# Performance work log

Measured on AMD Instinct MI355X. Metric: run time of the kernel, lower is better.

The kernel has to match this reference:

```python
import jax, jax.numpy as jnp
import numpy as np

HIDSZ = 256
NAGENTS = 8
NMODELS = 64
NACTIONS = 16
BN = 256  # batch * nagents
IN_DIM = 2 * HIDSZ
INIT_STD = 0.2


def setup_inputs() -> dict:
    key = jax.random.key(0)
    ks = jax.random.split(key, 12)
    inp = jax.random.normal(ks[0], (BN, IN_DIM), jnp.float32)
    prev_hid = jax.random.normal(ks[1], (BN, HIDSZ), jnp.float32)
    comm_in = jax.random.normal(ks[2], (BN, NAGENTS, HIDSZ), jnp.float32)
    agent_ids = jax.random.randint(ks[3], (BN,), 0, NMODELS)
    s = INIT_STD
    params = {
        'enc_w': jax.random.normal(ks[4], (IN_DIM, HIDSZ), jnp.float32) * s,
        'enc_b': jnp.zeros((HIDSZ,), jnp.float32),
        'rnn_w': jax.random.normal(ks[5], (NMODELS, HIDSZ, HIDSZ), jnp.float32) * s,
        'rnn_b': jnp.zeros((NMODELS, HIDSZ), jnp.float32),
        'act_w': jax.random.normal(ks[6], (NMODELS, HIDSZ, NACTIONS), jnp.float32) * s,
        'act_b': jnp.zeros((NMODELS, NACTIONS), jnp.float32),
        'base_w': jax.random.normal(ks[7], (NMODELS, HIDSZ, 1), jnp.float32) * s,
        'base_b': jnp.zeros((NMODELS, 1), jnp.float32),
        'comm_w': jax.random.normal(ks[8], (NMODELS, HIDSZ, HIDSZ * NAGENTS), jnp.float32) * s,
        'comm_b': jnp.zeros((NMODELS, HIDSZ * NAGENTS), jnp.float32),
    }
    return dict(inp=inp, prev_hid=prev_hid, comm_in=comm_in, agent_ids=agent_ids, **params)


def linear_multi(x, w_lut, b_lut, ids):
    # per-example (model-indexed) weight gather + batched matvec
    W = w_lut[ids]            # [BN, in, out]
    b = b_lut[ids]            # [BN, out]
    return jnp.einsum('bi,bio->bo', x, W) + b


def reference(inp, prev_hid, comm_in, agent_ids,
              enc_w, enc_b, rnn_w, rnn_b,
              act_w, act_b, base_w, base_b,
              comm_w, comm_b):
    # __comm2hid: sum over incoming agents (comm_encoder=0 -> identity)
    comm_ = jnp.sum(comm_in, axis=1)                            # [BN, hidsz]
    # _rnn: relu(enc(inp) + rnn_linear(prev_hid, ids) + comm_)
    pre = (inp @ enc_w + enc_b
           + linear_multi(prev_hid, rnn_w, rnn_b, agent_ids)
           + comm_)
    hid = jax.nn.relu(pre)                                      # [BN, hidsz]
    # __action: shared hidden -> policy + baseline
    action_prob = jax.nn.softmax(
        linear_multi(hid, act_w, act_b, agent_ids), axis=-1)    # [BN, nactions]
    baseline = linear_multi(hid, base_w, base_b, agent_ids)     # [BN, 1]
    # __comm_out (fully_connected=True)
    comm_out = linear_multi(hid, comm_w, comm_b, agent_ids)     # [BN, hidsz*nagents]
    return action_prob, baseline, hid, comm_out
```

## Files before the change

### kernel.cpp

```cpp
#include <hip/hip_runtime.h>

#define HIDSZ 256
#define NAGENTS 8
#define NMODELS 64
#define NACTIONS 16
#define BN 256
#define IN_DIM 512
#define COMMSZ 2048

#define OUT_ACT 0
#define OUT_BASE (BN * NACTIONS)
#define OUT_HID (OUT_BASE + BN)
#define OUT_COMM (OUT_HID + BN * HIDSZ)

__global__ void k_sort(const int* __restrict__ ids,
                       int* __restrict__ model_start,
                       int* __restrict__ row_of) {
    __shared__ int cnt[NMODELS];
    __shared__ int base[NMODELS + 1];
    int t = threadIdx.x;
    if (t < NMODELS) cnt[t] = 0;
    __syncthreads();
    int id = ids[t];
    atomicAdd(&cnt[id], 1);
    __syncthreads();
    if (t == 0) {
        int s = 0;
        for (int m = 0; m < NMODELS; ++m) { base[m] = s; s += cnt[m]; }
        base[NMODELS] = s;
    }
    __syncthreads();
    if (t <= NMODELS) model_start[t] = base[t];
    __syncthreads();
    int pos = atomicAdd(&base[id], 1);
    row_of[pos] = t;
}

__global__ __launch_bounds__(256) void k_hid(
    const float* __restrict__ inp, const float* __restrict__ prev_hid,
    const float* __restrict__ comm_in,
    const float* __restrict__ enc_w, const float* __restrict__ enc_b,
    const float* __restrict__ rnn_w, const float* __restrict__ rnn_b,
    const int* __restrict__ model_start, const int* __restrict__ row_of,
    float* __restrict__ out)
{
    int m = blockIdx.x;
    int s = model_start[m];
    int R = model_start[m + 1] - s;
    if (R == 0) return;
    int t = threadIdx.x, lane = t & 63, w = t >> 6;

    __shared__ float4 xs4[4][192];
    __shared__ float red[4][4][HIDSZ];

    for (int g = blockIdx.y; g * 4 < R; g += gridDim.y) {
        __syncthreads();
        {
            int ri = g * 4 + w;
            float4 z4 = make_float4(0.f, 0.f, 0.f, 0.f);
            if (ri < R) {
                int b = row_of[s + ri];
                const float4* ip = (const float4*)(inp + (size_t)b * IN_DIM);
                const float4* ph = (const float4*)(prev_hid + (size_t)b * HIDSZ);
                xs4[w][lane]       = ip[lane];
                xs4[w][64 + lane]  = ip[64 + lane];
                xs4[w][128 + lane] = ph[lane];
            } else {
                xs4[w][lane] = z4; xs4[w][64 + lane] = z4; xs4[w][128 + lane] = z4;
            }
        }
        __syncthreads();

        float acc[4][4];
        #pragma unroll
        for (int r = 0; r < 4; ++r)
            acc[r][0] = acc[r][1] = acc[r][2] = acc[r][3] = 0.f;

        const float* xs = (const float*)xs4;
        const float4* ew4 = (const float4*)enc_w;

        for (int i0 = 0; i0 < 128; i0 += 16) {
            float4 wv[16];
            #pragma unroll
            for (int u = 0; u < 16; ++u)
                wv[u] = ew4[(size_t)(128 * w + i0 + u) * 64 + lane];
            #pragma unroll
            for (int u = 0; u < 16; ++u) {
                int i = 128 * w + i0 + u;
                #pragma unroll
                for (int r = 0; r < 4; ++r) {
                    float x = xs[r * 768 + i];
                    acc[r][0] += x * wv[u].x; acc[r][1] += x * wv[u].y;
                    acc[r][2] += x * wv[u].z; acc[r][3] += x * wv[u].w;
                }
            }
        }
        const float4* rw4 = (const float4*)(rnn_w + (size_t)m * HIDSZ * HIDSZ);
        for (int i0 = 0; i0 < 64; i0 += 16) {
            float4 wv[16];
            #pragma unroll
            for (int u = 0; u < 16; ++u)
                wv[u] = rw4[(size_t)(64 * w + i0 + u) * 64 + lane];
            #pragma unroll
            for (int u = 0; u < 16; ++u) {
                int i = 64 * w + i0 + u;
                #pragma unroll
                for (int r = 0; r < 4; ++r) {
                    float x = xs[r * 768 + 512 + i];
                    acc[r][0] += x * wv[u].x; acc[r][1] += x * wv[u].y;
                    acc[r][2] += x * wv[u].z; acc[r][3] += x * wv[u].w;
                }
            }
        }
        #pragma unroll
        for (int r = 0; r < 4; ++r)
            *(float4*)&red[w][r][lane * 4] =
                make_float4(acc[r][0], acc[r][1], acc[r][2], acc[r][3]);
        __syncthreads();

        int ri = g * 4 + w;
        if (ri < R) {
            int b = row_of[s + ri];
            float4 s0 = *(const float4*)&red[0][w][lane * 4];
            float4 s1 = *(const float4*)&red[1][w][lane * 4];
            float4 s2 = *(const float4*)&red[2][w][lane * 4];
            float4 s3 = *(const float4*)&red[3][w][lane * 4];
            float4 cs = make_float4(0.f, 0.f, 0.f, 0.f);
            const float4* ci = (const float4*)(comm_in + (size_t)b * NAGENTS * HIDSZ);
            #pragma unroll
            for (int a = 0; a < NAGENTS; ++a) {
                float4 v = ci[a * 64 + lane];
                cs.x += v.x; cs.y += v.y; cs.z += v.z; cs.w += v.w;
            }
            float4 eb = ((const float4*)enc_b)[lane];
            float4 rb = ((const float4*)(rnn_b + m * HIDSZ))[lane];
            float4 h;
            h.x = fmaxf(s0.x + s1.x + s2.x + s3.x + cs.x + eb.x + rb.x, 0.f);
            h.y = fmaxf(s0.y + s1.y + s2.y + s3.y + cs.y + eb.y + rb.y, 0.f);
            h.z = fmaxf(s0.z + s1.z + s2.z + s3.z + cs.z + eb.z + rb.z, 0.f);
            h.w = fmaxf(s0.w + s1.w + s2.w + s3.w + cs.w + eb.w + rb.w, 0.f);
            ((float4*)(out + OUT_HID))[(size_t)b * 64 + lane] = h;
        }
    }
}

__global__ __launch_bounds__(256) void k_out(
    const float* __restrict__ act_w, const float* __restrict__ act_b,
    const float* __restrict__ base_w, const float* __restrict__ base_b,
    const float* __restrict__ comm_w, const float* __restrict__ comm_b,
    const int* __restrict__ model_start, const int* __restrict__ row_of,
    float* __restrict__ out)
{
    int m = blockIdx.x, y = blockIdx.y;
    int s = model_start[m];
    int R = model_start[m + 1] - s;
    if (R == 0) return;
    int t = threadIdx.x;
    const float* hid = out + OUT_HID;
    __shared__ float hs[16][HIDSZ];

    if (y == 4) {
        if (blockIdx.z != 0) return;
        const float* aw = act_w + m * HIDSZ * NACTIONS;
        const float* bw = base_w + m * HIDSZ;
        for (int g = 0; g * 16 < R; ++g) {
            __syncthreads();
            for (int k = t; k < 16 * 64; k += 256) {
                int rr = k >> 6, l = k & 63;
                int ri = g * 16 + rr;
                float4 v = make_float4(0.f, 0.f, 0.f, 0.f);
                if (ri < R) v = ((const float4*)(hid + (size_t)row_of[s + ri] * HIDSZ))[l];
                ((float4*)hs)[rr * 64 + l] = v;
            }
            __syncthreads();
            {
                int o = t & 15, rs = t >> 4;
                int ri = g * 16 + rs;
                if (ri < R) {
                    int b = row_of[s + ri];
                    float acc = act_b[m * NACTIONS + o];
                    #pragma unroll 8
                    for (int i = 0; i < HIDSZ; ++i)
                        acc += hs[rs][i] * aw[i * NACTIONS + o];
                    float mx = acc;
                    #pragma unroll
                    for (int d = 1; d < 16; d <<= 1) mx = fmaxf(mx, __shfl_xor(mx, d, 64));
                    float ex = __expf(acc - mx);
                    float sm = ex;
                    #pragma unroll
                    for (int d = 1; d < 16; d <<= 1) sm += __shfl_xor(sm, d, 64);
                    out[OUT_ACT + b * NACTIONS + o] = ex / sm;
                }
            }
            {
                int lane = t & 63, w = t >> 6;
                for (int rr = w; rr < 16; rr += 4) {
                    int ri = g * 16 + rr;
                    if (ri < R) {
                        int b = row_of[s + ri];
                        float p = 0.f;
                        #pragma unroll
                        for (int i = lane; i < HIDSZ; i += 64)
                            p += hs[rr][i] * bw[i];
                        #pragma unroll
                        for (int d = 1; d < 64; d <<= 1) p += __shfl_xor(p, d, 64);
                        if (lane == 0) out[OUT_BASE + b] = p + base_b[m];
                    }
                }
            }
        }
        return;
    }

    int cp = y * 256 + t;
    const float2* cw2 = (const float2*)(comm_w + (size_t)m * HIDSZ * COMMSZ);
    float2 cb = ((const float2*)(comm_b + (size_t)m * COMMSZ))[cp];

    for (int g = blockIdx.z; g * 8 < R; g += gridDim.z) {
        __syncthreads();
        for (int k = t; k < 8 * 64; k += 256) {
            int rr = k >> 6, l = k & 63;
            int ri = g * 8 + rr;
            float4 v = make_float4(0.f, 0.f, 0.f, 0.f);
            if (ri < R) v = ((const float4*)(hid + (size_t)row_of[s + ri] * HIDSZ))[l];
            ((float4*)hs)[rr * 64 + l] = v;
        }
        __syncthreads();

        float acc[8][2];
        #pragma unroll
        for (int r = 0; r < 8; ++r) { acc[r][0] = 0.f; acc[r][1] = 0.f; }

        for (int i0 = 0; i0 < HIDSZ; i0 += 16) {
            float2 wv[16];
            #pragma unroll
            for (int u = 0; u < 16; ++u)
                wv[u] = cw2[(size_t)(i0 + u) * 1024 + cp];
            #pragma unroll
            for (int u = 0; u < 16; ++u) {
                #pragma unroll
                for (int r = 0; r < 8; ++r) {
                    float h = hs[r][i0 + u];
                    acc[r][0] += h * wv[u].x;
                    acc[r][1] += h * wv[u].y;
                }
            }
        }
        #pragma unroll
        for (int r = 0; r < 8; ++r) {
            int ri = g * 8 + r;
            if (ri < R) {
                int b = row_of[s + ri];
                float2 o2;
                o2.x = acc[r][0] + cb.x;
                o2.y = acc[r][1] + cb.y;
                ((float2*)(out + OUT_COMM))[(size_t)b * 1024 + cp] = o2;
            }
        }
    }
}

extern "C" void kernel_launch(void* const* d_in, const int* in_sizes, int n_in,
                              void* d_out, int out_size, void* d_ws, size_t ws_size,
                              hipStream_t stream) {
    const float* inp      = (const float*)d_in[0];
    const float* prev_hid = (const float*)d_in[1];
    const float* comm_in  = (const float*)d_in[2];
    const int*   ids      = (const int*)d_in[3];
    const float* enc_w    = (const float*)d_in[4];
    const float* enc_b    = (const float*)d_in[5];
    const float* rnn_w    = (const float*)d_in[6];
    const float* rnn_b    = (const float*)d_in[7];
    const float* act_w    = (const float*)d_in[8];
    const float* act_b    = (const float*)d_in[9];
    const float* base_w   = (const float*)d_in[10];
    const float* base_b   = (const float*)d_in[11];
    const float* comm_w   = (const float*)d_in[12];
    const float* comm_b   = (const float*)d_in[13];
    float* out = (float*)d_out;

    int* model_start = (int*)d_ws;
    int* row_of      = model_start + 72;

    hipLaunchKernelGGL(k_sort, dim3(1), dim3(256), 0, stream,
                       ids, model_start, row_of);
    hipLaunchKernelGGL(k_hid, dim3(64, 2), dim3(256), 0, stream,
                       inp, prev_hid, comm_in, enc_w, enc_b, rnn_w, rnn_b,
                       model_start, row_of, out);
    hipLaunchKernelGGL(k_out, dim3(64, 5, 2), dim3(256), 0, stream,
                       act_w, act_b, base_w, base_b, comm_w, comm_b,
                       model_start, row_of, out);
}
```

Baseline: 280.2 us.

## Drop sort kernel, build per-model row lists in-block and split hid by column

Removes the single-block sort kernel; each block now scans the 256 agent ids and collects its own model's rows in shared memory. k_hid is restructured so blockIdx.y splits the 256 output columns into two halves instead of splitting row groups. Each thread covers a float2 column pair across 8 rows, and the K dimension is split across 4 waves and reduced through shared memory. This drops one launch and the dependency on the sort kernel, and halves per-block weight traffic in k_hid. The cost is that every block repeats the id scan.

```diff
diff --git a/kernel.cpp b/kernel.cpp
--- a/kernel.cpp
+++ b/kernel.cpp
@@ -6,6 +6,7 @@
 #define NACTIONS 16
 #define BN 256
 #define IN_DIM 512
+#define XDIM 768
 #define COMMSZ 2048
 
 #define OUT_ACT 0
@@ -13,27 +14,14 @@
 #define OUT_HID (OUT_BASE + BN)
 #define OUT_COMM (OUT_HID + BN * HIDSZ)
 
-__global__ void k_sort(const int* __restrict__ ids,
-                       int* __restrict__ model_start,
-                       int* __restrict__ row_of) {
-    __shared__ int cnt[NMODELS];
-    __shared__ int base[NMODELS + 1];
-    int t = threadIdx.x;
-    if (t < NMODELS) cnt[t] = 0;
+__device__ __forceinline__ int block_rows(const int* __restrict__ ids, int m,
+                                          int* rows, int* cnt, int t) {
+    if (t == 0) *cnt = 0;
     __syncthreads();
     int id = ids[t];
-    atomicAdd(&cnt[id], 1);
+    if (id == m) { int p = atomicAdd(cnt, 1); rows[p] = t; }
     __syncthreads();
-    if (t == 0) {
-        int s = 0;
-        for (int m = 0; m < NMODELS; ++m) { base[m] = s; s += cnt[m]; }
-        base[NMODELS] = s;
-    }
-    __syncthreads();
-    if (t <= NMODELS) model_start[t] = base[t];
-    __syncthreads();
-    int pos = atomicAdd(&base[id], 1);
-    row_of[pos] = t;
+    return *cnt;
 }
 
 __global__ __launch_bounds__(256) void k_hid(
@@ -41,105 +29,94 @@
     const float* __restrict__ comm_in,
     const float* __restrict__ enc_w, const float* __restrict__ enc_b,
     const float* __restrict__ rnn_w, const float* __restrict__ rnn_b,
-    const int* __restrict__ model_start, const int* __restrict__ row_of,
-    float* __restrict__ out)
+    const int* __restrict__ ids, float* __restrict__ out)
 {
-    int m = blockIdx.x;
-    int s = model_start[m];
-    int R = model_start[m + 1] - s;
+    int m = blockIdx.x, ch = blockIdx.y;
+    __shared__ int rows[BN];
+    __shared__ int cnt;
+    int t = threadIdx.x;
+    int R = block_rows(ids, m, rows, &cnt, t);
     if (R == 0) return;
-    int t = threadIdx.x, lane = t & 63, w = t >> 6;
-
-    __shared__ float4 xs4[4][192];
-    __shared__ float red[4][4][HIDSZ];
-
-    for (int g = blockIdx.y; g * 4 < R; g += gridDim.y) {
-        __syncthreads();
-        {
-            int ri = g * 4 + w;
-            float4 z4 = make_float4(0.f, 0.f, 0.f, 0.f);
+
+    __shared__ float xs[8][XDIM];
+    __shared__ float red[4][8][128];
+
+    int cp = t & 63;
+    int sl = t >> 6;
+    int cbase = ch * 128;
+    const float2* ew2 = (const float2*)enc_w;
+    const float2* rw2 = (const float2*)(rnn_w + (size_t)m * HIDSZ * HIDSZ);
+
+    for (int g = 0; g * 8 < R; ++g) {
+        __syncthreads();
+        for (int j = t; j < 8 * 192; j += 256) {
+            int r = j / 192, q = j % 192;
+            int ri = g * 8 + r;
+            float4 v = make_float4(0.f, 0.f, 0.f, 0.f);
             if (ri < R) {
-                int b = row_of[s + ri];
-                const float4* ip = (const float4*)(inp + (size_t)b * IN_DIM);
-                const float4* ph = (const float4*)(prev_hid + (size_t)b * HIDSZ);
-                xs4[w][lane]       = ip[lane];
-                xs4[w][64 + lane]  = ip[64 + lane];
-                xs4[w][128 + lane] = ph[lane];
-            } else {
-                xs4[w][lane] = z4; xs4[w][64 + lane] = z4; xs4[w][128 + lane] = z4;
-            }
-        }
-        __syncthreads();
-
-        float acc[4][4];
-        #pragma unroll
-        for (int r = 0; r < 4; ++r)
-            acc[r][0] = acc[r][1] = acc[r][2] = acc[r][3] = 0.f;
-
-        const float* xs = (const float*)xs4;
-        const float4* ew4 = (const float4*)enc_w;
-
-        for (int i0 = 0; i0 < 128; i0 += 16) {
-            float4 wv[16];
-            #pragma unroll
-            for (int u = 0; u < 16; ++u)
-                wv[u] = ew4[(size_t)(128 * w + i0 + u) * 64 + lane];
+                int b = rows[ri];
+                v = (q < 128) ? ((const float4*)(inp + (size_t)b * IN_DIM))[q]
+                              : ((const float4*)(prev_hid + (size_t)b * HIDSZ))[q - 128];
+            }
+            ((float4*)xs)[j] = v;
+        }
+        __syncthreads();
+
+        float a0[8], a1[8];
+        #pragma unroll
+        for (int r = 0; r < 8; ++r) { a0[r] = 0.f; a1[r] = 0.f; }
+
+        int ibase = sl * 192;
+        for (int i0 = 0; i0 < 192; i0 += 16) {
+            float2 wv[16];
             #pragma unroll
             for (int u = 0; u < 16; ++u) {
-                int i = 128 * w + i0 + u;
-                #pragma unroll
-                for (int r = 0; r < 4; ++r) {
-                    float x = xs[r * 768 + i];
-                    acc[r][0] += x * wv[u].x; acc[r][1] += x * wv[u].y;
-                    acc[r][2] += x * wv[u].z; acc[r][3] += x * wv[u].w;
-                }
-            }
-        }
-        const float4* rw4 = (const float4*)(rnn_w + (size_t)m * HIDSZ * HIDSZ);
-        for (int i0 = 0; i0 < 64; i0 += 16) {
-            float4 wv[16];
-            #pragma unroll
-            for (int u = 0; u < 16; ++u)
-                wv[u] = rw4[(size_t)(64 * w + i0 + u) * 64 + lane];
+                int i = ibase + i0 + u;
+                wv[u] = (i < IN_DIM) ? ew2[(size_t)i * 128 + ch * 64 + cp]
+                                     : rw2[(size_t)(i - IN_DIM) * 128 + ch * 64 + cp];
+            }
             #pragma unroll
             for (int u = 0; u < 16; ++u) {
-                int i = 64 * w + i0 + u;
-                #pragma unroll
-                for (int r = 0; r < 4; ++r) {
-                    float x = xs[r * 768 + 512 + i];
-                    acc[r][0] += x * wv[u].x; acc[r][1] += x * wv[u].y;
-                    acc[r][2] += x * wv[u].z; acc[r][3] += x * wv[u].w;
-                }
-            }
-        }
-        #pragma unroll
-        for (int r = 0; r < 4; ++r)
-            *(float4*)&red[w][r][lane * 4] =
-                make_float4(acc[r][0], acc[r][1], acc[r][2], acc[r][3]);
-        __syncthreads();
-
-        int ri = g * 4 + w;
-        if (ri < R) {
-            int b = row_of[s + ri];
-            float4 s0 = *(const float4*)&red[0][w][lane * 4];
-            float4 s1 = *(const float4*)&red[1][w][lane * 4];
-            float4 s2 = *(const float4*)&red[2][w][lane * 4];
-            float4 s3 = *(const float4*)&red[3][w][lane * 4];
-            float4 cs = make_float4(0.f, 0.f, 0.f, 0.f);
-            const float4* ci = (const float4*)(comm_in + (size_t)b * NAGENTS * HIDSZ);
-            #pragma unroll
-            for (int a = 0; a < NAGENTS; ++a) {
-                float4 v = ci[a * 64 + lane];
-                cs.x += v.x; cs.y += v.y; cs.z += v.z; cs.w += v.w;
-            }
-            float4 eb = ((const float4*)enc_b)[lane];
-            float4 rb = ((const float4*)(rnn_b + m * HIDSZ))[lane];
-            float4 h;
-            h.x = fmaxf(s0.x + s1.x + s2.x + s3.x + cs.x + eb.x + rb.x, 0.f);
-            h.y = fmaxf(s0.y + s1.y + s2.y + s3.y + cs.y + eb.y + rb.y, 0.f);
-            h.z = fmaxf(s0.z + s1.z + s2.z + s3.z + cs.z + eb.z + rb.z, 0.f);
-            h.w = fmaxf(s0.w + s1.w + s2.w + s3.w + cs.w + eb.w + rb.w, 0.f);
-            ((float4*)(out + OUT_HID))[(size_t)b * 64 + lane] = h;
+                int i = ibase + i0 + u;
+                #pragma unroll
+                for (int r = 0; r < 8; ++r) {
+                    float x = xs[r][i];
+                    a0[r] += x * wv[u].x;
+                    a1[r] += x * wv[u].y;
+                }
+            }
+        }
+        #pragma unroll
+        for (int r = 0; r < 8; ++r)
+            *(float2*)&red[sl][r][cp * 2] = make_float2(a0[r], a1[r]);
+        __syncthreads();
+
+        for (int j = t; j < 512; j += 256) {
+            int r = j >> 6, q = j & 63;
+            int ri = g * 8 + r;
+            if (ri < R) {
+                int b = rows[ri];
+                float2 s = make_float2(0.f, 0.f);
+                #pragma unroll
+                for (int s4 = 0; s4 < 4; ++s4) {
+                    float2 p = *(const float2*)&red[s4][r][q * 2];
+                    s.x += p.x; s.y += p.y;
+                }
+                int c = cbase + q * 2;
+                const float2* ci = (const float2*)(comm_in + (size_t)b * NAGENTS * HIDSZ);
+                float2 cs = make_float2(0.f, 0.f);
+                #pragma unroll
+                for (int a = 0; a < NAGENTS; ++a) {
+                    float2 v = ci[a * (HIDSZ / 2) + (c >> 1)];
+                    cs.x += v.x; cs.y += v.y;
+                }
+                float2 eb = *(const float2*)(enc_b + c);
+                float2 rb = *(const float2*)(rnn_b + m * HIDSZ + c);
+                float2 h;
+                h.x = fmaxf(s.x + cs.x + eb.x + rb.x, 0.f);
+                h.y = fmaxf(s.y + cs.y + eb.y + rb.y, 0.f);
+                *(float2*)(out + OUT_HID + (size_t)b * HIDSZ + c) = h;
+            }
         }
     }
 }
@@ -148,14 +125,14 @@
     const float* __restrict__ act_w, const float* __restrict__ act_b,
     const float* __restrict__ base_w, const float* __restrict__ base_b,
     const float* __restrict__ comm_w, const float* __restrict__ comm_b,
-    const int* __restrict__ model_start, const int* __restrict__ row_of,
-    float* __restrict__ out)
+    const int* __restrict__ ids, float* __restrict__ out)
 {
     int m = blockIdx.x, y = blockIdx.y;
-    int s = model_start[m];
-    int R = model_start[m + 1] - s;
+    __shared__ int rows[BN];
+    __shared__ int cnt;
+    int t = threadIdx.x;
+    int R = block_rows(ids, m, rows, &cnt, t);
     if (R == 0) return;
-    int t = threadIdx.x;
     const float* hid = out + OUT_HID;
     __shared__ float hs[16][HIDSZ];
 
@@ -169,7 +146,7 @@
                 int rr = k >> 6, l = k & 63;
                 int ri = g * 16 + rr;
                 float4 v = make_float4(0.f, 0.f, 0.f, 0.f);
-                if (ri < R) v = ((const float4*)(hid + (size_t)row_of[s + ri] * HIDSZ))[l];
+                if (ri < R) v = ((const float4*)(hid + (size_t)rows[ri] * HIDSZ))[l];
                 ((float4*)hs)[rr * 64 + l] = v;
             }
             __syncthreads();
@@ -177,7 +154,7 @@
                 int o = t & 15, rs = t >> 4;
                 int ri = g * 16 + rs;
                 if (ri < R) {
-                    int b = row_of[s + ri];
+                    int b = rows[ri];
                     float acc = act_b[m * NACTIONS + o];
                     #pragma unroll 8
                     for (int i = 0; i < HIDSZ; ++i)
@@ -197,7 +174,7 @@
                 for (int rr = w; rr < 16; rr += 4) {
                     int ri = g * 16 + rr;
                     if (ri < R) {
-                        int b = row_of[s + ri];
+                        int b = rows[ri];
                         float p = 0.f;
                         #pragma unroll
                         for (int i = lane; i < HIDSZ; i += 64)
@@ -222,7 +199,7 @@
             int rr = k >> 6, l = k & 63;
             int ri = g * 8 + rr;
             float4 v = make_float4(0.f, 0.f, 0.f, 0.f);
-            if (ri < R) v = ((const float4*)(hid + (size_t)row_of[s + ri] * HIDSZ))[l];
+            if (ri < R) v = ((const float4*)(hid + (size_t)rows[ri] * HIDSZ))[l];
             ((float4*)hs)[rr * 64 + l] = v;
         }
         __syncthreads();
@@ -250,7 +227,7 @@
         for (int r = 0; r < 8; ++r) {
             int ri = g * 8 + r;
             if (ri < R) {
-                int b = row_of[s + ri];
+                int b = rows[ri];
                 float2 o2;
                 o2.x = acc[r][0] + cb.x;
                 o2.y = acc[r][1] + cb.y;
@@ -279,15 +256,10 @@
     const float* comm_b   = (const float*)d_in[13];
     float* out = (float*)d_out;
 
-    int* model_start = (int*)d_ws;
-    int* row_of      = model_start + 72;
-
-    hipLaunchKernelGGL(k_sort, dim3(1), dim3(256), 0, stream,
-                       ids, model_start, row_of);
     hipLaunchKernelGGL(k_hid, dim3(64, 2), dim3(256), 0, stream,
                        inp, prev_hid, comm_in, enc_w, enc_b, rnn_w, rnn_b,
-                       model_start, row_of, out);
+                       ids, out);
     hipLaunchKernelGGL(k_out, dim3(64, 5, 2), dim3(256), 0, stream,
                        act_w, act_b, base_w, base_b, comm_w, comm_b,
-                       model_start, row_of, out);
-}
+                       ids, out);
+}
```

Result: faster. 249.5 us (-11.0%).
